# Performance work log

Measured on AMD Instinct MI355X. Metric: run time of the kernel, lower is better.

The kernel has to match this reference:

```python
import jax, jax.numpy as jnp
import numpy as np

N = 8192      # nodes
E = 16384     # query edges
D = 256       # node feature dim
NNZ = 262144  # overlap matrix nnz (avg degree 32)
P1, P2, P3 = 32, 32, 32


def _mlp(x, W1, b1, W2, b2):
    # Linear(1->p) -> ReLU -> Linear(p->1)
    return jax.nn.relu(x @ W1 + b1) @ W2 + b2


def setup_inputs() -> dict:
    key = jax.random.key(0)
    ks = jax.random.split(key, 16)
    inp = {
        "edges": jax.random.randint(ks[0], (E, 2), 0, N, dtype=jnp.int32),
        "row": jax.random.randint(ks[1], (NNZ,), 0, N, dtype=jnp.int32),
        "col": jax.random.randint(ks[2], (NNZ,), 0, N, dtype=jnp.int32),
        "values": jax.random.uniform(ks[3], (NNZ,), dtype=jnp.float32),
        "H": jax.random.normal(ks[4], (N, D), dtype=jnp.float32),
        # f_edge: 1 -> P1 -> 1
        "we1": jax.random.normal(ks[5], (1, P1), dtype=jnp.float32) * 0.5,
        "be1": jnp.zeros((P1,), jnp.float32),
        "we2": jax.random.normal(ks[6], (P1, 1), dtype=jnp.float32) * 0.5,
        "be2": jnp.zeros((1,), jnp.float32),
        # f_node: 1 -> P2 -> 1
        "wn1": jax.random.normal(ks[7], (1, P2), dtype=jnp.float32) * 0.5,
        "bn1": jnp.zeros((P2,), jnp.float32),
        "wn2": jax.random.normal(ks[8], (P2, 1), dtype=jnp.float32) * 0.5,
        "bn2": jnp.zeros((1,), jnp.float32),
        # psi_3: 1 -> P3 -> 1
        "wp1": jax.random.normal(ks[9], (1, P3), dtype=jnp.float32) * 0.5,
        "bp1": jnp.zeros((P3,), jnp.float32),
        "wp2": jax.random.normal(ks[10], (P3, 1), dtype=jnp.float32) * 0.5,
        "bp2": jnp.zeros((1,), jnp.float32),
        "alpha": jnp.zeros((2,), jnp.float32),
    }
    return inp


def reference(edges, row, col, values, H,
              we1, be1, we2, be2,
              wn1, bn1, wn2, bn2,
              wp1, bp1, wp2, bp2, alpha):
    src, dst = edges[:, 0], edges[:, 1]

    # --- BatchDotPred: sigmoid(<H[src], H[dst]>) ---
    h_link = jax.nn.sigmoid(jnp.einsum('ed,ed->e', H[src], H[dst]))[:, None]  # [E,1]

    # --- MultiHopAggregator ---
    edge_feat = _mlp(values[:, None], we1, be1, we2, be2)           # [NNZ,1]
    node_in = jax.ops.segment_sum(edge_feat, col, num_segments=N)  # [N,1] scatter_add over col
    struct = _mlp(node_in, wn1, bn1, wn2, bn2)[:, 0]                # [N]

    # dense overlap adjacency (coo.todense(), duplicates summed)
    adj = jnp.zeros((N, N), values.dtype).at[row, col].add(values)  # [N,N]

    # NOTE: faithful to source bug: both src and dst neighborhoods gather src rows
    sn = adj[src]                                                   # [E,N]
    agg = jnp.einsum('en,n->e', sn * sn, struct * struct)[:, None]  # [E,1]

    z_link = jax.nn.sigmoid(_mlp(agg, wp1, bp1, wp2, bp2))          # [E,1]

    a = jax.nn.softmax(alpha)
    y_hat = a[0] * z_link + a[1] * h_link + 1e-15
    return y_hat
```

## Files before the change

kernel.cpp:

```cpp
#include <hip/hip_runtime.h>
#include <math.h>

#define N_NODES 8192
#define D_DIM   256
#define E_EDGES 16384
#define NNZ_CNT 262144


#define NBLK_A 128
#define BT     1024
#define NNZ_PB (NNZ_CNT / NBLK_A)
#define EDG_PB (E_EDGES / NBLK_A)

__device__ __forceinline__ float sigmoidf(float x) {
    return 1.0f / (1.0f + expf(-x));
}


__global__ __launch_bounds__(BT) void k_stage(
    const int* __restrict__ col, const float* __restrict__ values,
    const int* __restrict__ edges, const float* __restrict__ H,
    const float* __restrict__ we1, const float* __restrict__ be1,
    const float* __restrict__ we2, const float* __restrict__ be2,
    float* __restrict__ partial, float* __restrict__ hbuf)
{
    __shared__ float bins[N_NODES];
    const int tid = threadIdx.x;
    const int bid = blockIdx.x;
    for (int j = tid; j < N_NODES; j += BT) bins[j] = 0.0f;
    __syncthreads();

    int base = bid * NNZ_PB;
#pragma unroll
    for (int it = 0; it < NNZ_PB / BT; ++it) {
        int k = base + it * BT + tid;
        float v = values[k];
        int c = col[k];
        float f = be2[0];
#pragma unroll
        for (int j = 0; j < 32; ++j) {
            float t = fmaf(v, we1[j], be1[j]);
            t = t > 0.0f ? t : 0.0f;
            f = fmaf(t, we2[j], f);
        }
        atomicAdd(&bins[c], f);
    }

    {
        int wave = tid >> 6, lane = tid & 63;
        const float4* H4 = (const float4*)H;
#pragma unroll
        for (int i = 0; i < EDG_PB / 16; ++i) {
            int e = bid * EDG_PB + wave * (EDG_PB / 16) + i;
            int src = edges[2 * e];
            int dst = edges[2 * e + 1];
            float4 a4 = H4[src * (D_DIM / 4) + lane];
            float4 b4 = H4[dst * (D_DIM / 4) + lane];
            float dot = a4.x * b4.x + a4.y * b4.y + a4.z * b4.z + a4.w * b4.w;
#pragma unroll
            for (int off = 32; off >= 1; off >>= 1)
                dot += __shfl_xor(dot, off, 64);
            if (lane == 0) hbuf[e] = sigmoidf(dot);
        }
    }

    __syncthreads();
    float* p = partial + (size_t)bid * N_NODES;
    for (int j = tid; j < N_NODES; j += BT) p[j] = bins[j];
}

__global__ __launch_bounds__(BT) void k_node(
    const float* __restrict__ partial,
    const float* __restrict__ wn1, const float* __restrict__ bn1,
    const float* __restrict__ wn2, const float* __restrict__ bn2,
    float* __restrict__ struct2, float* __restrict__ racc)
{
    __shared__ float red[BT];
    const int tid = threadIdx.x;
    const int sub = tid & 127;
    const int g   = tid >> 7;
    int i = blockIdx.x * 128 + sub;
    float x = 0.0f;
#pragma unroll
    for (int j = 0; j < 16; ++j)
        x += partial[(size_t)(g * 16 + j) * N_NODES + i];
    red[tid] = x;
    __syncthreads();
    if (tid < 128) {
        int i2 = blockIdx.x * 128 + tid;
        float s = 0.0f;
#pragma unroll
        for (int b = 0; b < 8; ++b) s += red[b * 128 + tid];
        float u = bn2[0];
#pragma unroll
        for (int j = 0; j < 32; ++j) {
            float t = fmaf(s, wn1[j], bn1[j]);
            t = t > 0.0f ? t : 0.0f;
            u = fmaf(t, wn2[j], u);
        }
        struct2[i2] = u * u;
        racc[i2] = 0.0f;
    }
}

__global__ __launch_bounds__(BT) void k_racc(
    const int* __restrict__ row, const int* __restrict__ col,
    const float* __restrict__ values, const float* __restrict__ struct2,
    float* __restrict__ racc)
{
    int k = blockIdx.x * BT + threadIdx.x;
    float v = values[k];
    atomicAdd(&racc[row[k]], v * v * struct2[col[k]]);
}

__global__ __launch_bounds__(BT) void k_final(
    const int* __restrict__ edges, const float* __restrict__ racc,
    const float* __restrict__ hbuf,
    const float* __restrict__ wp1, const float* __restrict__ bp1,
    const float* __restrict__ wp2, const float* __restrict__ bp2,
    const float* __restrict__ alpha, float* __restrict__ out)
{
    int e = blockIdx.x * BT + threadIdx.x;
    int src = edges[2 * e];
    float agg = racc[src];
    float u = bp2[0];
#pragma unroll
    for (int j = 0; j < 32; ++j) {
        float t = fmaf(agg, wp1[j], bp1[j]);
        t = t > 0.0f ? t : 0.0f;
        u = fmaf(t, wp2[j], u);
    }
    float z = sigmoidf(u);
    float h = hbuf[e];
    float a0 = alpha[0], a1 = alpha[1];
    float m = fmaxf(a0, a1);
    float e0 = expf(a0 - m);
    float e1 = expf(a1 - m);
    float inv = 1.0f / (e0 + e1);
    out[e] = (e0 * inv) * z + (e1 * inv) * h + 1e-15f;
}

extern "C" void kernel_launch(void* const* d_in, const int* in_sizes, int n_in,
                              void* d_out, int out_size, void* d_ws, size_t ws_size,
                              hipStream_t stream) {
    const int*   edges  = (const int*)d_in[0];
    const int*   row    = (const int*)d_in[1];
    const int*   col    = (const int*)d_in[2];
    const float* values = (const float*)d_in[3];
    const float* H      = (const float*)d_in[4];
    const float* we1    = (const float*)d_in[5];
    const float* be1    = (const float*)d_in[6];
    const float* we2    = (const float*)d_in[7];
    const float* be2    = (const float*)d_in[8];
    const float* wn1    = (const float*)d_in[9];
    const float* bn1    = (const float*)d_in[10];
    const float* wn2    = (const float*)d_in[11];
    const float* bn2    = (const float*)d_in[12];
    const float* wp1    = (const float*)d_in[13];
    const float* bp1    = (const float*)d_in[14];
    const float* wp2    = (const float*)d_in[15];
    const float* bp2    = (const float*)d_in[16];
    const float* alpha  = (const float*)d_in[17];
    float* outf = (float*)d_out;

    float* ws_f    = (float*)d_ws;
    float* partial = ws_f;
    float* struct2 = ws_f + (size_t)NBLK_A * N_NODES;
    float* racc    = struct2 + N_NODES;
    float* hbuf    = racc + N_NODES;

    k_stage<<<NBLK_A, BT, 0, stream>>>(col, values, edges, H,
                                       we1, be1, we2, be2, partial, hbuf);
    k_node<<<N_NODES / 128, BT, 0, stream>>>(partial, wn1, bn1, wn2, bn2,
                                             struct2, racc);
    k_racc<<<NNZ_CNT / BT, BT, 0, stream>>>(row, col, values, struct2, racc);
    k_final<<<E_EDGES / BT, BT, 0, stream>>>(edges, racc, hbuf,
                                             wp1, bp1, wp2, bp2, alpha, outf);
}
```

Before: 129.9 us.

## Fuse racc and final kernels via last-block ticket, widen stage grid

Moves the racc zeroing into the first kernel and merges the scatter into racc with the final per-edge MLP. A global ticket counter lets only the last finishing block compute all outputs. The first kernel now runs 256 blocks with one nnz per thread, and the node reduction is reshaped to 32 nodes per block across 256 blocks. This drops one launch and raises parallelism in the first stage. In exchange, the partial buffer doubles to 256 rows per node and the final 16K-edge epilogue is serialized into a single block.

```diff
diff --git a/kernel.cpp b/kernel.cpp
--- a/kernel.cpp
+++ b/kernel.cpp
@@ -7,33 +7,32 @@
 #define NNZ_CNT 262144
 
 
-#define NBLK_A 128
-#define BT     1024
-#define NNZ_PB (NNZ_CNT / NBLK_A)
-#define EDG_PB (E_EDGES / NBLK_A)
+#define NB 256
+#define BT 1024
 
 __device__ __forceinline__ float sigmoidf(float x) {
     return 1.0f / (1.0f + expf(-x));
 }
-
 
 __global__ __launch_bounds__(BT) void k_stage(
     const int* __restrict__ col, const float* __restrict__ values,
     const int* __restrict__ edges, const float* __restrict__ H,
     const float* __restrict__ we1, const float* __restrict__ be1,
     const float* __restrict__ we2, const float* __restrict__ be2,
-    float* __restrict__ partial, float* __restrict__ hbuf)
+    float* __restrict__ partial, float* __restrict__ hbuf,
+    float* __restrict__ racc, unsigned int* __restrict__ counter)
 {
     __shared__ float bins[N_NODES];
     const int tid = threadIdx.x;
     const int bid = blockIdx.x;
+#pragma unroll
     for (int j = tid; j < N_NODES; j += BT) bins[j] = 0.0f;
+    if (tid < 32) racc[bid * 32 + tid] = 0.0f;
+    if (bid == 0 && tid == 0) *counter = 0u;
     __syncthreads();
 
-    int base = bid * NNZ_PB;
-#pragma unroll
-    for (int it = 0; it < NNZ_PB / BT; ++it) {
-        int k = base + it * BT + tid;
+    {
+        int k = bid * BT + tid;
         float v = values[k];
         int c = col[k];
         float f = be2[0];
@@ -50,8 +49,8 @@
         int wave = tid >> 6, lane = tid & 63;
         const float4* H4 = (const float4*)H;
 #pragma unroll
-        for (int i = 0; i < EDG_PB / 16; ++i) {
-            int e = bid * EDG_PB + wave * (EDG_PB / 16) + i;
+        for (int i = 0; i < 4; ++i) {
+            int e = bid * 64 + wave * 4 + i;
             int src = edges[2 * e];
             int dst = edges[2 * e + 1];
             float4 a4 = H4[src * (D_DIM / 4) + lane];
@@ -66,6 +65,7 @@
 
     __syncthreads();
     float* p = partial + (size_t)bid * N_NODES;
+#pragma unroll
     for (int j = tid; j < N_NODES; j += BT) p[j] = bins[j];
 }
 
@@ -73,24 +73,24 @@
     const float* __restrict__ partial,
     const float* __restrict__ wn1, const float* __restrict__ bn1,
     const float* __restrict__ wn2, const float* __restrict__ bn2,
-    float* __restrict__ struct2, float* __restrict__ racc)
+    float* __restrict__ struct2)
 {
-    __shared__ float red[BT];
-    const int tid = threadIdx.x;
-    const int sub = tid & 127;
-    const int g   = tid >> 7;
-    int i = blockIdx.x * 128 + sub;
+    __shared__ float red[32 * 33];
+    const int tid  = threadIdx.x;
+    const int lane = tid & 31;
+    const int g    = tid >> 5;
+    int i = blockIdx.x * 32 + lane;
     float x = 0.0f;
 #pragma unroll
-    for (int j = 0; j < 16; ++j)
-        x += partial[(size_t)(g * 16 + j) * N_NODES + i];
-    red[tid] = x;
+    for (int j = 0; j < 8; ++j)
+        x += partial[(size_t)(g * 8 + j) * N_NODES + i];
+    red[g * 33 + lane] = x;
     __syncthreads();
-    if (tid < 128) {
-        int i2 = blockIdx.x * 128 + tid;
+    if (tid < 32) {
+        int i2 = blockIdx.x * 32 + tid;
         float s = 0.0f;
 #pragma unroll
-        for (int b = 0; b < 8; ++b) s += red[b * 128 + tid];
+        for (int g2 = 0; g2 < 32; ++g2) s += red[g2 * 33 + tid];
         float u = bn2[0];
 #pragma unroll
         for (int j = 0; j < 32; ++j) {
@@ -99,45 +99,54 @@
             u = fmaf(t, wn2[j], u);
         }
         struct2[i2] = u * u;
-        racc[i2] = 0.0f;
     }
 }
 
-__global__ __launch_bounds__(BT) void k_racc(
+__global__ __launch_bounds__(BT) void k_racc_final(
     const int* __restrict__ row, const int* __restrict__ col,
     const float* __restrict__ values, const float* __restrict__ struct2,
-    float* __restrict__ racc)
-{
-    int k = blockIdx.x * BT + threadIdx.x;
-    float v = values[k];
-    atomicAdd(&racc[row[k]], v * v * struct2[col[k]]);
-}
-
-__global__ __launch_bounds__(BT) void k_final(
-    const int* __restrict__ edges, const float* __restrict__ racc,
-    const float* __restrict__ hbuf,
+    const int* __restrict__ edges, const float* __restrict__ hbuf,
     const float* __restrict__ wp1, const float* __restrict__ bp1,
     const float* __restrict__ wp2, const float* __restrict__ bp2,
-    const float* __restrict__ alpha, float* __restrict__ out)
+    const float* __restrict__ alpha,
+    float* __restrict__ racc, unsigned int* __restrict__ counter,
+    float* __restrict__ out)
 {
-    int e = blockIdx.x * BT + threadIdx.x;
-    int src = edges[2 * e];
-    float agg = racc[src];
-    float u = bp2[0];
+    const int tid = threadIdx.x;
+    const int bid = blockIdx.x;
+    {
+        int k = bid * BT + tid;
+        float v = values[k];
+        atomicAdd(&racc[row[k]], v * v * struct2[col[k]]);
+    }
+    __threadfence();
+    __syncthreads();
+    __shared__ unsigned int ticket;
+    if (tid == 0) ticket = atomicAdd(counter, 1u);
+    __syncthreads();
+    if (ticket != NB - 1) return;
+    __threadfence();
+
+    float a0 = alpha[0], a1 = alpha[1];
+    float m  = fmaxf(a0, a1);
+    float e0 = expf(a0 - m), e1 = expf(a1 - m);
+    float inv = 1.0f / (e0 + e1);
 #pragma unroll
-    for (int j = 0; j < 32; ++j) {
-        float t = fmaf(agg, wp1[j], bp1[j]);
-        t = t > 0.0f ? t : 0.0f;
-        u = fmaf(t, wp2[j], u);
+    for (int i = 0; i < E_EDGES / BT; ++i) {
+        int e = i * BT + tid;
+        int src = edges[2 * e];
+        float agg = __hip_atomic_load(&racc[src], __ATOMIC_RELAXED,
+                                      __HIP_MEMORY_SCOPE_AGENT);
+        float u = bp2[0];
+#pragma unroll
+        for (int j = 0; j < 32; ++j) {
+            float t = fmaf(agg, wp1[j], bp1[j]);
+            t = t > 0.0f ? t : 0.0f;
+            u = fmaf(t, wp2[j], u);
+        }
+        float z = sigmoidf(u);
+        out[e] = (e0 * inv) * z + (e1 * inv) * hbuf[e] + 1e-15f;
     }
-    float z = sigmoidf(u);
-    float h = hbuf[e];
-    float a0 = alpha[0], a1 = alpha[1];
-    float m = fmaxf(a0, a1);
-    float e0 = expf(a0 - m);
-    float e1 = expf(a1 - m);
-    float inv = 1.0f / (e0 + e1);
-    out[e] = (e0 * inv) * z + (e1 * inv) * h + 1e-15f;
 }
 
 extern "C" void kernel_launch(void* const* d_in, const int* in_sizes, int n_in,
@@ -165,15 +174,16 @@
 
     float* ws_f    = (float*)d_ws;
     float* partial = ws_f;
-    float* struct2 = ws_f + (size_t)NBLK_A * N_NODES;
+    float* struct2 = ws_f + (size_t)NB * N_NODES;
     float* racc    = struct2 + N_NODES;
     float* hbuf    = racc + N_NODES;
+    unsigned int* counter = (unsigned int*)(hbuf + E_EDGES);
 
-    k_stage<<<NBLK_A, BT, 0, stream>>>(col, values, edges, H,
-                                       we1, be1, we2, be2, partial, hbuf);
-    k_node<<<N_NODES / 128, BT, 0, stream>>>(partial, wn1, bn1, wn2, bn2,
-                                             struct2, racc);
-    k_racc<<<NNZ_CNT / BT, BT, 0, stream>>>(row, col, values, struct2, racc);
-    k_final<<<E_EDGES / BT, BT, 0, stream>>>(edges, racc, hbuf,
-                                             wp1, bp1, wp2, bp2, alpha, outf);
+    k_stage<<<NB, BT, 0, stream>>>(col, values, edges, H,
+                                   we1, be1, we2, be2,
+                                   partial, hbuf, racc, counter);
+    k_node<<<NB, BT, 0, stream>>>(partial, wn1, bn1, wn2, bn2, struct2);
+    k_racc_final<<<NB, BT, 0, stream>>>(row, col, values, struct2,
+                                        edges, hbuf, wp1, bp1, wp2, bp2,
+                                        alpha, racc, counter, outf);
 }
```

Result: slower. 194.9 us (+50.1%).
